# Kernel tuning notes

Measured on AMD Instinct MI355X. Metric: run time of the kernel, lower is better.

Reference implementation:

```python
import jax, jax.numpy as jnp
import numpy as np

EPS = 1e-12  # matches torch F.normalize eps


def _l2n(x, axis):
    return x / jnp.maximum(jnp.linalg.norm(x, axis=axis, keepdims=True), EPS)


def setup_inputs() -> dict:
    key = jax.random.key(0)
    k1, k2, k3 = jax.random.split(key, 3)
    x = jax.random.normal(k1, (4, 128, 30, 40), dtype=jnp.float32)
    conv_w = jax.random.normal(k2, (64, 128), dtype=jnp.float32) * 0.02  # 1x1 conv, no bias (vladv2=False)
    centroids = jax.random.uniform(k3, (64, 128), dtype=jnp.float32)
    return {"x": x, "conv_w": conv_w, "centroids": centroids}


def reference(x, conv_w, centroids):
    N, C, H, W = x.shape
    K = centroids.shape[0]
    ps, stride = 4, 1  # patch_sizes='4', strides='1'

    # descriptor-wise L2 normalization of input
    x = _l2n(x, 1)

    # 1x1 conv + softmax over clusters -> soft assignment [N,K,H,W]
    soft_assign = jax.nn.softmax(jnp.einsum('kc,nchw->nkhw', conv_w, x), axis=1)

    # weighted residuals [N,K,C,H,W] (vectorized form of the per-cluster loop)
    res = (x[:, None] - centroids[None, :, :, None, None]) * soft_assign[:, :, None]

    # global VLAD: sum over spatial, intra-norm, flatten, L2-norm
    vlad_global = res.sum(axis=(-1, -2))            # [N,K,C]
    vlad_global = _l2n(vlad_global, 2).reshape(N, K * C)
    vlad_global = _l2n(vlad_global, 1)

    # integral image over spatial dims with zero pad on top/left
    r = res.reshape(N, K * C, H, W)
    integ = jnp.cumsum(jnp.cumsum(r, axis=-1), axis=-2)
    integ = jnp.pad(integ, ((0, 0), (0, 0), (1, 0), (1, 0)))  # [N,KC,H+1,W+1]

    # dilated 2x2 box-filter conv == 4-corner integral-image lookup
    TL = integ[:, :, :H + 1 - ps:stride, :W + 1 - ps:stride]
    TR = integ[:, :, :H + 1 - ps:stride, ps::stride]
    BL = integ[:, :, ps::stride, :W + 1 - ps:stride]
    BR = integ[:, :, ps::stride, ps::stride]
    vl = (TL - TR - BL + BR) / (ps * ps)            # [N,KC,Hp,Wp]
    Hp, Wp = vl.shape[-2], vl.shape[-1]

    # local VLAD: intra-norm over descriptor dim, then global L2 per patch
    vl = vl.reshape(N, K, C, Hp * Wp)
    vl = _l2n(vl, 2).reshape(N, K * C, Hp * Wp)
    vlad_local = _l2n(vl, 1)

    return vlad_global, vlad_local
```

## Files before the change

kernel.cpp:

```cpp
#include <hip/hip_runtime.h>
#include <math.h>

#define EPSV 1e-12f

namespace {
constexpr int N_  = 4;
constexpr int C_  = 128;
constexpr int H_  = 30;
constexpr int W_  = 40;
constexpr int K_  = 64;
constexpr int HW_ = H_ * W_;
constexpr int HP_ = 27;
constexpr int WP_ = 37;
constexpr int P_  = HP_ * WP_;
constexpr int KC_ = K_ * C_;
constexpr int CP_ = C_ * P_;
constexpr int CS_ = HP_ * W_;
constexpr int SL_ = CS_ / 4;
}

static __device__ __forceinline__ float4 ld4(const float* p) {
    return *reinterpret_cast<const float4*>(p);
}

__global__ __launch_bounds__(256) void k1_norm_softmax(
    const float* __restrict__ x, const float* __restrict__ conv_w,
    float* __restrict__ xnT, float* __restrict__ xnP, float* __restrict__ sa)
{
    __shared__ float xrow[C_ * W_];
    __shared__ float conv_s[K_ * C_];
    __shared__ float invn[W_];
    __shared__ float s_s[K_ * W_];

    const int b = blockIdx.x;
    const int n = b / H_, h = b - n * H_;
    const int t = threadIdx.x;

    for (int i = t; i < C_ * W_; i += 256) {
        const int c = i / W_, w = i - c * W_;
        xrow[i] = x[(size_t)(n * C_ + c) * HW_ + h * W_ + w];
    }
    for (int i = t; i < K_ * C_; i += 256) conv_s[i] = conv_w[i];
    __syncthreads();

    if (t < W_) {
        float s = 0.f;
        for (int c = 0; c < C_; ++c) { const float v = xrow[c * W_ + t]; s += v * v; }
        invn[t] = 1.f / fmaxf(sqrtf(s), EPSV);
    }
    __syncthreads();

    for (int i = t; i < C_ * W_; i += 256) {
        const int c = i / W_, w = i - c * W_;
        const float v = xrow[i] * invn[w];
        xrow[i] = v;
        xnT[(size_t)(n * C_ + c) * HW_ + h * W_ + w] = v;
    }
    __syncthreads();

    for (int i = t; i < W_ * C_; i += 256) {
        const int w = i / C_, c = i - w * C_;
        xnP[((size_t)n * HW_ + h * W_ + w) * C_ + c] = xrow[c * W_ + w];
    }

    for (int d = t; d < K_ * W_; d += 256) {
        const int k = d / W_, w = d - k * W_;
        const float* cw = &conv_s[k * C_];
        float s = 0.f;
        for (int c = 0; c < C_; ++c) s += cw[c] * xrow[c * W_ + w];
        s_s[d] = s;
    }
    __syncthreads();

    if (t < W_) {
        const int w = t;
        float m = -1e30f;
        for (int k = 0; k < K_; ++k) m = fmaxf(m, s_s[k * W_ + w]);
        float sum = 0.f;
        for (int k = 0; k < K_; ++k) sum += expf(s_s[k * W_ + w] - m);
        const float inv = 1.f / sum;
        for (int k = 0; k < K_; ++k)
            sa[(size_t)(n * K_ + k) * HW_ + h * W_ + w] = expf(s_s[k * W_ + w] - m) * inv;
    }
}

#define COLSUM_VEC_T(cs_q, sa_s, x0, x1, x2, x3)                                \
    for (int s = t; s < SL_; s += 256) {                                        \
        const int i = s * 4;                                                    \
        const float4 sa0 = ld4(&sa_s[i]);                                       \
        const float4 sa1 = ld4(&sa_s[i + W_]);                                  \
        const float4 sa2 = ld4(&sa_s[i + 2 * W_]);                              \
        const float4 sa3 = ld4(&sa_s[i + 3 * W_]);                              \
        float acc[4][4];                                                        \
        const float* xc[4] = {x0, x1, x2, x3};                                  \
        _Pragma("unroll")                                                       \
        for (int ch = 0; ch < 4; ++ch) {                                        \
            const float4 a0 = ld4(xc[ch] + i);                                  \
            const float4 a1 = ld4(xc[ch] + i + W_);                             \
            const float4 a2 = ld4(xc[ch] + i + 2 * W_);                         \
            const float4 a3 = ld4(xc[ch] + i + 3 * W_);                         \
            acc[0][ch] = sa0.x * a0.x + sa1.x * a1.x + sa2.x * a2.x + sa3.x * a3.x; \
            acc[1][ch] = sa0.y * a0.y + sa1.y * a1.y + sa2.y * a2.y + sa3.y * a3.y; \
            acc[2][ch] = sa0.z * a0.z + sa1.z * a1.z + sa2.z * a2.z + sa3.z * a3.z; \
            acc[3][ch] = sa0.w * a0.w + sa1.w * a1.w + sa2.w * a2.w + sa3.w * a3.w; \
        }                                                                       \
        _Pragma("unroll")                                                       \
        for (int q = 0; q < 4; ++q)                                             \
            cs_q[q][s] = make_float4(acc[q][0], acc[q][1], acc[q][2], acc[q][3]); \
    }

static __device__ __forceinline__ float4 csget(const float4 cs_q[4][SL_], int e) {
    return cs_q[e & 3][e >> 2];
}

__global__ __launch_bounds__(256) void k4_merged(
    const float* __restrict__ sa, const float* __restrict__ xnT,
    const float* __restrict__ xnP, const float* __restrict__ cent,
    float* __restrict__ nsqp, float* __restrict__ vg_u,
    float* __restrict__ vg_r)
{
    __shared__ float  sa_s[HW_];
    __shared__ float  B_s[P_];
    __shared__ float4 cs_q[4][SL_];
    __shared__ float  gs[256], bss[256];
    __shared__ float  red[2];

    const int t = threadIdx.x;

    if (blockIdx.x < 256) {
        const int b = blockIdx.x;
        const int n = b >> 6, k = b & 63;
        const int c = t & 127, half = t >> 7;
        constexpr int HHW = HW_ / 2;

        const float* sarow = &sa[(size_t)b * HW_ + half * HHW];
        const float* xp = &xnP[((size_t)n * HW_ + half * HHW) * C_ + c];
        float g0 = 0.f, g1 = 0.f, g2 = 0.f, g3 = 0.f;
        float b0 = 0.f, b1 = 0.f, b2 = 0.f, b3 = 0.f;
        for (int pix = 0; pix < HHW; pix += 4) {
            const float s0 = sarow[pix + 0], s1 = sarow[pix + 1];
            const float s2 = sarow[pix + 2], s3 = sarow[pix + 3];
            g0 += s0 * xp[(size_t)(pix + 0) * C_];
            g1 += s1 * xp[(size_t)(pix + 1) * C_];
            g2 += s2 * xp[(size_t)(pix + 2) * C_];
            g3 += s3 * xp[(size_t)(pix + 3) * C_];
            b0 += s0; b1 += s1; b2 += s2; b3 += s3;
        }
        gs[t]  = (g0 + g1) + (g2 + g3);
        bss[t] = (b0 + b1) + (b2 + b3);
        __syncthreads();

        float vg = 0.f;
        if (t < 128) {
            vg = (gs[t] + gs[t + 128]) - cent[k * C_ + c] * (bss[t] + bss[t + 128]);
            float nsq = vg * vg;
            for (int off = 32; off >= 1; off >>= 1) nsq += __shfl_down(nsq, off);
            if ((t & 63) == 0) red[t >> 6] = nsq;
        }
        __syncthreads();
        const float tot  = red[0] + red[1];
        const float norm = sqrtf(tot);
        const float iv   = 1.f / fmaxf(norm, EPSV);
        if (t < 128) vg_u[(size_t)b * C_ + t] = vg * iv;
        if (t == 0) { const float rr = norm * iv; vg_r[b] = rr * rr; }
        return;
    }

    const int b  = blockIdx.x - 256;
    const int cq = b & 3;
    const int nk = b >> 2;
    const int n  = nk >> 6, k = nk & 63;

    for (int i = t; i < HW_; i += 256) sa_s[i] = sa[(size_t)nk * HW_ + i];
    __syncthreads();
    for (int p = t; p < P_; p += 256) {
        const int hp = p / WP_, wp = p - hp * WP_;
        float bs = 0.f;
#pragma unroll
        for (int dh = 0; dh < 4; ++dh) {
            const float* r = &sa_s[(hp + dh) * W_ + wp];
            bs += r[0] + r[1] + r[2] + r[3];
        }
        B_s[p] = bs;
    }

    float nsq0 = 0.f, nsq1 = 0.f, nsq2 = 0.f, nsq3 = 0.f;
    const float* xb = xnT + (size_t)n * C_ * HW_;

    for (int g = 0; g < 8; ++g) {
        const int c0 = cq * 32 + g * 4;
        const float* x0 = xb + (size_t)(c0 + 0) * HW_;
        const float* x1 = xb + (size_t)(c0 + 1) * HW_;
        const float* x2 = xb + (size_t)(c0 + 2) * HW_;
        const float* x3 = xb + (size_t)(c0 + 3) * HW_;
        __syncthreads();
        COLSUM_VEC_T(cs_q, sa_s, x0, x1, x2, x3)
        __syncthreads();
        const float4 ce = ld4(&cent[k * C_ + c0]);
#pragma unroll
        for (int pi = 0; pi < 4; ++pi) {
            const int p = t + pi * 256;
            if (p < P_) {
                const int hp = p / WP_, wp = p - hp * WP_;
                const int base = hp * W_ + wp;
                const float4 s0 = csget(cs_q, base);
                const float4 s1 = csget(cs_q, base + 1);
                const float4 s2 = csget(cs_q, base + 2);
                const float4 s3 = csget(cs_q, base + 3);
                const float Bv = B_s[p];
                const float ux = (s0.x + s1.x + s2.x + s3.x) - ce.x * Bv;
                const float uy = (s0.y + s1.y + s2.y + s3.y) - ce.y * Bv;
                const float uz = (s0.z + s1.z + s2.z + s3.z) - ce.z * Bv;
                const float uw = (s0.w + s1.w + s2.w + s3.w) - ce.w * Bv;
                const float add = ux * ux + uy * uy + uz * uz + uw * uw;
                if      (pi == 0) nsq0 += add;
                else if (pi == 1) nsq1 += add;
                else if (pi == 2) nsq2 += add;
                else              nsq3 += add;
            }
        }
    }
#pragma unroll
    for (int pi = 0; pi < 4; ++pi) {
        const int p = t + pi * 256;
        if (p < P_) {
            const float v = (pi == 0 ? nsq0 : pi == 1 ? nsq1 : pi == 2 ? nsq2 : nsq3);
            nsqp[(size_t)b * P_ + p] = v * 0.00390625f;
        }
    }
}

__global__ __launch_bounds__(256) void k5_merged(
    const float* __restrict__ nsqp, float* __restrict__ inv1,
    float* __restrict__ rloc, const float* __restrict__ vg_u,
    const float* __restrict__ vg_r, float* __restrict__ out)
{
    const int t = threadIdx.x;
    if (blockIdx.x >= 256) {
        const int n = blockIdx.x - 256;
        __shared__ float inv2s;
        if (t == 0) {
            float s = 0.f;
            for (int k = 0; k < K_; ++k) s += vg_r[n * K_ + k];
            inv2s = 1.f / fmaxf(sqrtf(s), EPSV);
        }
        __syncthreads();
        const float inv2 = inv2s;
        for (int i = t; i < KC_; i += 256)
            out[(size_t)n * KC_ + i] = vg_u[(size_t)n * KC_ + i] * inv2;
        return;
    }
    const int nk = blockIdx.x;
    for (int p = t; p < P_; p += 256) {
        const float s = nsqp[(size_t)(nk * 4 + 0) * P_ + p]
                      + nsqp[(size_t)(nk * 4 + 1) * P_ + p]
                      + nsqp[(size_t)(nk * 4 + 2) * P_ + p]
                      + nsqp[(size_t)(nk * 4 + 3) * P_ + p];
        const float norm = sqrtf(s);
        const float iv = 1.f / fmaxf(norm, EPSV);
        inv1[(size_t)nk * P_ + p] = iv * 0.0625f;
        const float rr = norm * iv;
        rloc[(size_t)nk * P_ + p] = rr * rr;
    }
}

__global__ __launch_bounds__(256) void k6_inv2(
    const float* __restrict__ rloc, float* __restrict__ inv2)
{
    const int n = blockIdx.x >> 2;
    const int p = (blockIdx.x & 3) * 256 + threadIdx.x;
    if (p < P_) {
        float s = 0.f;
        for (int k = 0; k < K_; ++k) s += rloc[(size_t)(n * K_ + k) * P_ + p];
        inv2[n * P_ + p] = 1.f / fmaxf(sqrtf(s), EPSV);
    }
}

__global__ __launch_bounds__(256) void k7_write(
    const float* __restrict__ sa, const float* __restrict__ xnT,
    const float* __restrict__ cent, const float* __restrict__ inv1,
    const float* __restrict__ inv2, float* __restrict__ outl)
{
    __shared__ float  sa_s[HW_];
    __shared__ float  scl_s[P_];
    __shared__ float  t2_s[P_];
    __shared__ float4 cs_q[4][SL_];

    const int b  = blockIdx.x;
    const int cq = b & 3;
    const int nk = b >> 2;
    const int n  = nk >> 6, k = nk & 63;
    const int t  = threadIdx.x;

    for (int i = t; i < HW_; i += 256) sa_s[i] = sa[(size_t)nk * HW_ + i];
    __syncthreads();
    for (int p = t; p < P_; p += 256) {
        const int hp = p / WP_, wp = p - hp * WP_;
        float bs = 0.f;
#pragma unroll
        for (int dh = 0; dh < 4; ++dh) {
            const float* r = &sa_s[(hp + dh) * W_ + wp];
            bs += r[0] + r[1] + r[2] + r[3];
        }
        const float sc = inv1[(size_t)nk * P_ + p] * inv2[n * P_ + p];
        scl_s[p] = sc;
        t2_s[p]  = bs * sc;
    }

    const float* xb = xnT + (size_t)n * C_ * HW_;
    float* ob = outl + (size_t)nk * CP_;

    for (int g = 0; g < 8; ++g) {
        const int m = g & 3, h8 = g >> 2;
        const int c0 = cq * 32 + h8 * 16 + m;
        const float* x0 = xb + (size_t)(c0 + 0) * HW_;
        const float* x1 = xb + (size_t)(c0 + 4) * HW_;
        const float* x2 = xb + (size_t)(c0 + 8) * HW_;
        const float* x3 = xb + (size_t)(c0 + 12) * HW_;
        __syncthreads();
        COLSUM_VEC_T(cs_q, sa_s, x0, x1, x2, x3)
        __syncthreads();
        const float ce0 = cent[k * C_ + c0];
        const float ce1 = cent[k * C_ + c0 + 4];
        const float ce2 = cent[k * C_ + c0 + 8];
        const float ce3 = cent[k * C_ + c0 + 12];
        float* ob0 = ob + (size_t)(c0 + 0) * P_;
        float* ob1 = ob + (size_t)(c0 + 4) * P_;
        float* ob2 = ob + (size_t)(c0 + 8) * P_;
        float* ob3 = ob + (size_t)(c0 + 12) * P_;

        if (t < 249) {
            const int p0 = m + t * 4;
            float4 v0, v1, v2, v3;
#pragma unroll
            for (int pi = 0; pi < 4; ++pi) {
                const int p = p0 + pi;
                const int hp = p / WP_, wp = p - hp * WP_;
                const int base = hp * W_ + wp;
                const float4 s0 = csget(cs_q, base);
                const float4 s1 = csget(cs_q, base + 1);
                const float4 s2 = csget(cs_q, base + 2);
                const float4 s3 = csget(cs_q, base + 3);
                const float sc = scl_s[p], tt = t2_s[p];
                reinterpret_cast<float*>(&v0)[pi] = (s0.x + s1.x + s2.x + s3.x) * sc - ce0 * tt;
                reinterpret_cast<float*>(&v1)[pi] = (s0.y + s1.y + s2.y + s3.y) * sc - ce1 * tt;
                reinterpret_cast<float*>(&v2)[pi] = (s0.z + s1.z + s2.z + s3.z) * sc - ce2 * tt;
                reinterpret_cast<float*>(&v3)[pi] = (s0.w + s1.w + s2.w + s3.w) * sc - ce3 * tt;
            }
            *reinterpret_cast<float4*>(ob0 + p0) = v0;
            *reinterpret_cast<float4*>(ob1 + p0) = v1;
            *reinterpret_cast<float4*>(ob2 + p0) = v2;
            *reinterpret_cast<float4*>(ob3 + p0) = v3;
        } else if (t < 252) {
            const int u = t - 249;
            const int p = (u < m) ? u : 996 + u;
            const int hp = p / WP_, wp = p - hp * WP_;
            const int base = hp * W_ + wp;
            const float4 s0 = csget(cs_q, base);
            const float4 s1 = csget(cs_q, base + 1);
            const float4 s2 = csget(cs_q, base + 2);
            const float4 s3 = csget(cs_q, base + 3);
            const float sc = scl_s[p], tt = t2_s[p];
            ob0[p] = (s0.x + s1.x + s2.x + s3.x) * sc - ce0 * tt;
            ob1[p] = (s0.y + s1.y + s2.y + s3.y) * sc - ce1 * tt;
            ob2[p] = (s0.z + s1.z + s2.z + s3.z) * sc - ce2 * tt;
            ob3[p] = (s0.w + s1.w + s2.w + s3.w) * sc - ce3 * tt;
        }
    }
}

extern "C" void kernel_launch(void* const* d_in, const int* in_sizes, int n_in,
                              void* d_out, int out_size, void* d_ws, size_t ws_size,
                              hipStream_t stream)
{
    const float* x      = (const float*)d_in[0];
    const float* conv_w = (const float*)d_in[1];
    const float* cent   = (const float*)d_in[2];
    float* out = (float*)d_out;
    float* ws  = (float*)d_ws;

    float* xnT  = ws;
    float* xnP  = ws + 614400;
    float* sa   = ws + 1228800;
    float* vg_u = ws + 1536000;
    float* vg_r = ws + 1568768;
    float* nsqp = ws + 1569024;
    float* inv1 = ws + 2592000;
    float* rloc = ws + 2847744;
    float* inv2 = ws + 3103488;

    float* outl = out + (size_t)N_ * KC_;

    k1_norm_softmax<<<N_ * H_, 256, 0, stream>>>(x, conv_w, xnT, xnP, sa);
    k4_merged<<<256 + N_ * K_ * 4, 256, 0, stream>>>(sa, xnT, xnP, cent,
                                                     nsqp, vg_u, vg_r);
    k5_merged<<<256 + N_, 256, 0, stream>>>(nsqp, inv1, rloc, vg_u, vg_r, out);
    k6_inv2<<<N_ * 4, 256, 0, stream>>>(rloc, inv2);
    k7_write<<<N_ * K_ * 4, 256, 0, stream>>>(sa, xnT, cent, inv1, inv2, outl);
}
```

Baseline: 123.1 us.

## Share sliding box-filter windows across four patches per thread and vectorize intermediates

Each thread now computes four consecutive patch outputs from a 10-element window of column sums, sharing partial sums so fewer shared-memory reads are needed than with per-patch 4-tap gathers. The B box sums in k4 move into registers the same way. Intermediate per-patch buffers are padded to a stride of 1000 so they can be read and written as float4, and k6 drops to one block per batch. In k1 the 1x1 conv is restructured around a padded transposed tile for float4 dot products. The trade-offs are more register pressure and a select at row boundaries, and k6 now runs with far fewer blocks.

```diff
diff --git a/kernel.cpp b/kernel.cpp
--- a/kernel.cpp
+++ b/kernel.cpp
@@ -13,14 +13,22 @@
 constexpr int HP_ = 27;
 constexpr int WP_ = 37;
 constexpr int P_  = HP_ * WP_;
+constexpr int PS_ = 1000;
 constexpr int KC_ = K_ * C_;
 constexpr int CP_ = C_ * P_;
 constexpr int CS_ = HP_ * W_;
 constexpr int SL_ = CS_ / 4;
+constexpr int CVP_ = 132;
 }
 
 static __device__ __forceinline__ float4 ld4(const float* p) {
     return *reinterpret_cast<const float4*>(p);
+}
+static __device__ __forceinline__ float dot4(float4 a, float4 b) {
+    return a.x * b.x + a.y * b.y + a.z * b.z + a.w * b.w;
+}
+static __device__ __forceinline__ float4 f4add(float4 a, float4 b) {
+    return make_float4(a.x + b.x, a.y + b.y, a.z + b.z, a.w + b.w);
 }
 
 __global__ __launch_bounds__(256) void k1_norm_softmax(
@@ -28,7 +36,8 @@
     float* __restrict__ xnT, float* __restrict__ xnP, float* __restrict__ sa)
 {
     __shared__ float xrow[C_ * W_];
-    __shared__ float conv_s[K_ * C_];
+    __shared__ float conv_s[K_ * CVP_];
+    __shared__ float xrowT[W_ * CVP_];
     __shared__ float invn[W_];
     __shared__ float s_s[K_ * W_];
 
@@ -40,7 +49,10 @@
         const int c = i / W_, w = i - c * W_;
         xrow[i] = x[(size_t)(n * C_ + c) * HW_ + h * W_ + w];
     }
-    for (int i = t; i < K_ * C_; i += 256) conv_s[i] = conv_w[i];
+    for (int i = t; i < K_ * C_; i += 256) {
+        const int k = i >> 7, c = i & 127;
+        conv_s[k * CVP_ + c] = conv_w[i];
+    }
     __syncthreads();
 
     if (t < W_) {
@@ -60,15 +72,39 @@
 
     for (int i = t; i < W_ * C_; i += 256) {
         const int w = i / C_, c = i - w * C_;
-        xnP[((size_t)n * HW_ + h * W_ + w) * C_ + c] = xrow[c * W_ + w];
-    }
-
-    for (int d = t; d < K_ * W_; d += 256) {
-        const int k = d / W_, w = d - k * W_;
-        const float* cw = &conv_s[k * C_];
-        float s = 0.f;
-        for (int c = 0; c < C_; ++c) s += cw[c] * xrow[c * W_ + w];
-        s_s[d] = s;
+        const float v = xrow[c * W_ + w];
+        xnP[((size_t)n * HW_ + h * W_ + w) * C_ + c] = v;
+        xrowT[w * CVP_ + c] = v;
+    }
+    __syncthreads();
+
+    {
+        const int k = t >> 2, q = t & 3;
+        float acc0 = 0.f, acc1 = 0.f, acc2 = 0.f, acc3 = 0.f, acc4 = 0.f;
+        float acc5 = 0.f, acc6 = 0.f, acc7 = 0.f, acc8 = 0.f, acc9 = 0.f;
+        const float* convk = &conv_s[k * CVP_];
+        for (int ch = 0; ch < 4; ++ch) {
+            float4 cv0 = ld4(convk + ch * 32 + 0),  cv1 = ld4(convk + ch * 32 + 4);
+            float4 cv2 = ld4(convk + ch * 32 + 8),  cv3 = ld4(convk + ch * 32 + 12);
+            float4 cv4 = ld4(convk + ch * 32 + 16), cv5 = ld4(convk + ch * 32 + 20);
+            float4 cv6 = ld4(convk + ch * 32 + 24), cv7 = ld4(convk + ch * 32 + 28);
+#pragma unroll
+            for (int wi = 0; wi < 10; ++wi) {
+                const float* xw = &xrowT[(q * 10 + wi) * CVP_ + ch * 32];
+                float s = dot4(cv0, ld4(xw)) + dot4(cv1, ld4(xw + 4))
+                        + dot4(cv2, ld4(xw + 8)) + dot4(cv3, ld4(xw + 12))
+                        + dot4(cv4, ld4(xw + 16)) + dot4(cv5, ld4(xw + 20))
+                        + dot4(cv6, ld4(xw + 24)) + dot4(cv7, ld4(xw + 28));
+                if      (wi == 0) acc0 += s; else if (wi == 1) acc1 += s;
+                else if (wi == 2) acc2 += s; else if (wi == 3) acc3 += s;
+                else if (wi == 4) acc4 += s; else if (wi == 5) acc5 += s;
+                else if (wi == 6) acc6 += s; else if (wi == 7) acc7 += s;
+                else if (wi == 8) acc8 += s; else              acc9 += s;
+            }
+        }
+        float* sd = &s_s[k * W_ + q * 10];
+        sd[0] = acc0; sd[1] = acc1; sd[2] = acc2; sd[3] = acc3; sd[4] = acc4;
+        sd[5] = acc5; sd[6] = acc6; sd[7] = acc7; sd[8] = acc8; sd[9] = acc9;
     }
     __syncthreads();
 
@@ -109,9 +145,29 @@
             cs_q[q][s] = make_float4(acc[q][0], acc[q][1], acc[q][2], acc[q][3]); \
     }
 
-static __device__ __forceinline__ float4 csget(const float4 cs_q[4][SL_], int e) {
-    return cs_q[e & 3][e >> 2];
-}
+#define WINDOW10(cs_q, b0, d, A0, A1, A2, A3)                                   \
+    {                                                                           \
+        float4 v0 = cs_q[(b0 + 0) & 3][(b0 + 0) >> 2];                          \
+        float4 v1 = cs_q[(b0 + 1) & 3][(b0 + 1) >> 2];                          \
+        float4 v2 = cs_q[(b0 + 2) & 3][(b0 + 2) >> 2];                          \
+        float4 v3 = cs_q[(b0 + 3) & 3][(b0 + 3) >> 2];                          \
+        float4 v4 = cs_q[(b0 + 4) & 3][(b0 + 4) >> 2];                          \
+        float4 v5 = cs_q[(b0 + 5) & 3][(b0 + 5) >> 2];                          \
+        float4 v6 = cs_q[(b0 + 6) & 3][(b0 + 6) >> 2];                          \
+        float4 v7 = cs_q[(b0 + 7) & 3][(b0 + 7) >> 2];                          \
+        float4 v8 = cs_q[(b0 + 8) & 3][(b0 + 8) >> 2];                          \
+        float4 v9 = cs_q[(b0 + 9) & 3][(b0 + 9) >> 2];                          \
+        const float4 t0 = f4add(v0, v1), t1 = f4add(v1, v2), t2 = f4add(v2, v3);\
+        const float4 t3 = f4add(v3, v4), t4 = f4add(v4, v5), t5 = f4add(v5, v6);\
+        const float4 t6 = f4add(v6, v7), t7 = f4add(v7, v8), t8 = f4add(v8, v9);\
+        const float4 w0 = f4add(t0, t2), w1 = f4add(t1, t3), w2 = f4add(t2, t4);\
+        const float4 w3 = f4add(t3, t5), w4 = f4add(t4, t6), w5 = f4add(t5, t7);\
+        const float4 w6 = f4add(t6, t8);                                        \
+        A0 = (0 < d) ? w0 : w3;                                                 \
+        A1 = (1 < d) ? w1 : w4;                                                 \
+        A2 = (2 < d) ? w2 : w5;                                                 \
+        A3 = (3 < d) ? w3 : w6;                                                 \
+    }
 
 __global__ __launch_bounds__(256) void k4_merged(
     const float* __restrict__ sa, const float* __restrict__ xnT,
@@ -119,9 +175,8 @@
     float* __restrict__ nsqp, float* __restrict__ vg_u,
     float* __restrict__ vg_r)
 {
-    __shared__ float  sa_s[HW_];
-    __shared__ float  B_s[P_];
-    __shared__ float4 cs_q[4][SL_];
+    __shared__ float  sa_s[HW_ + 8];
+    __shared__ float4 cs_q[4][SL_ + 1];
     __shared__ float  gs[256], bss[256];
     __shared__ float  red[2];
 
@@ -173,18 +228,32 @@
 
     for (int i = t; i < HW_; i += 256) sa_s[i] = sa[(size_t)nk * HW_ + i];
     __syncthreads();
-    for (int p = t; p < P_; p += 256) {
-        const int hp = p / WP_, wp = p - hp * WP_;
-        float bs = 0.f;
+
+    int hp0 = 0, b0 = 0, d = 4;
+    float B0 = 0.f, B1 = 0.f, B2 = 0.f, B3 = 0.f;
+    if (t < 250) {
+        const int p0 = 4 * t;
+        hp0 = p0 / WP_;
+        const int wp0 = p0 - hp0 * WP_;
+        b0 = p0 + 3 * hp0;
+        d  = WP_ - wp0;
+        const float* r0 = &sa_s[hp0 * W_ + wp0];
+        float sc[10];
 #pragma unroll
-        for (int dh = 0; dh < 4; ++dh) {
-            const float* r = &sa_s[(hp + dh) * W_ + wp];
-            bs += r[0] + r[1] + r[2] + r[3];
-        }
-        B_s[p] = bs;
-    }
-
-    float nsq0 = 0.f, nsq1 = 0.f, nsq2 = 0.f, nsq3 = 0.f;
+        for (int j = 0; j < 10; ++j)
+            sc[j] = r0[j] + r0[j + W_] + r0[j + 2 * W_] + r0[j + 3 * W_];
+        const float u0 = sc[0] + sc[1], u1 = sc[1] + sc[2], u2 = sc[2] + sc[3];
+        const float u3 = sc[3] + sc[4], u4 = sc[4] + sc[5], u5 = sc[5] + sc[6];
+        const float u6 = sc[6] + sc[7], u7 = sc[7] + sc[8], u8 = sc[8] + sc[9];
+        const float wB0 = u0 + u2, wB1 = u1 + u3, wB2 = u2 + u4;
+        const float wB3 = u3 + u5, wB4 = u4 + u6, wB5 = u5 + u7, wB6 = u6 + u8;
+        B0 = (0 < d) ? wB0 : wB3;
+        B1 = (1 < d) ? wB1 : wB4;
+        B2 = (2 < d) ? wB2 : wB5;
+        B3 = (3 < d) ? wB3 : wB6;
+    }
+
+    float4 nv0 = make_float4(0, 0, 0, 0), nv1 = nv0, nv2 = nv0, nv3 = nv0;
     const float* xb = xnT + (size_t)n * C_ * HW_;
 
     for (int g = 0; g < 8; ++g) {
@@ -196,37 +265,36 @@
         __syncthreads();
         COLSUM_VEC_T(cs_q, sa_s, x0, x1, x2, x3)
         __syncthreads();
-        const float4 ce = ld4(&cent[k * C_ + c0]);
-#pragma unroll
-        for (int pi = 0; pi < 4; ++pi) {
-            const int p = t + pi * 256;
-            if (p < P_) {
-                const int hp = p / WP_, wp = p - hp * WP_;
-                const int base = hp * W_ + wp;
-                const float4 s0 = csget(cs_q, base);
-                const float4 s1 = csget(cs_q, base + 1);
-                const float4 s2 = csget(cs_q, base + 2);
-                const float4 s3 = csget(cs_q, base + 3);
-                const float Bv = B_s[p];
-                const float ux = (s0.x + s1.x + s2.x + s3.x) - ce.x * Bv;
-                const float uy = (s0.y + s1.y + s2.y + s3.y) - ce.y * Bv;
-                const float uz = (s0.z + s1.z + s2.z + s3.z) - ce.z * Bv;
-                const float uw = (s0.w + s1.w + s2.w + s3.w) - ce.w * Bv;
-                const float add = ux * ux + uy * uy + uz * uz + uw * uw;
-                if      (pi == 0) nsq0 += add;
-                else if (pi == 1) nsq1 += add;
-                else if (pi == 2) nsq2 += add;
-                else              nsq3 += add;
-            }
-        }
-    }
-#pragma unroll
-    for (int pi = 0; pi < 4; ++pi) {
-        const int p = t + pi * 256;
-        if (p < P_) {
-            const float v = (pi == 0 ? nsq0 : pi == 1 ? nsq1 : pi == 2 ? nsq2 : nsq3);
-            nsqp[(size_t)b * P_ + p] = v * 0.00390625f;
-        }
+        if (t < 250) {
+            const float4 ce = ld4(&cent[k * C_ + c0]);
+            float4 A0, A1, A2, A3;
+            WINDOW10(cs_q, b0, d, A0, A1, A2, A3)
+            const float4 e0 = make_float4(A0.x - ce.x * B0, A0.y - ce.y * B0,
+                                          A0.z - ce.z * B0, A0.w - ce.w * B0);
+            const float4 e1 = make_float4(A1.x - ce.x * B1, A1.y - ce.y * B1,
+                                          A1.z - ce.z * B1, A1.w - ce.w * B1);
+            const float4 e2 = make_float4(A2.x - ce.x * B2, A2.y - ce.y * B2,
+                                          A2.z - ce.z * B2, A2.w - ce.w * B2);
+            const float4 e3 = make_float4(A3.x - ce.x * B3, A3.y - ce.y * B3,
+                                          A3.z - ce.z * B3, A3.w - ce.w * B3);
+            nv0 = make_float4(nv0.x + e0.x * e0.x, nv0.y + e0.y * e0.y,
+                              nv0.z + e0.z * e0.z, nv0.w + e0.w * e0.w);
+            nv1 = make_float4(nv1.x + e1.x * e1.x, nv1.y + e1.y * e1.y,
+                              nv1.z + e1.z * e1.z, nv1.w + e1.w * e1.w);
+            nv2 = make_float4(nv2.x + e2.x * e2.x, nv2.y + e2.y * e2.y,
+                              nv2.z + e2.z * e2.z, nv2.w + e2.w * e2.w);
+            nv3 = make_float4(nv3.x + e3.x * e3.x, nv3.y + e3.y * e3.y,
+                              nv3.z + e3.z * e3.z, nv3.w + e3.w * e3.w);
+        }
+    }
+    if (t < 250) {
+        const float s0 = (nv0.x + nv0.y) + (nv0.z + nv0.w);
+        const float s1 = (nv1.x + nv1.y) + (nv1.z + nv1.w);
+        const float s2 = (nv2.x + nv2.y) + (nv2.z + nv2.w);
+        const float s3 = (nv3.x + nv3.y) + (nv3.z + nv3.w);
+        *reinterpret_cast<float4*>(&nsqp[(size_t)b * PS_ + 4 * t]) =
+            make_float4(s0 * 0.00390625f, s1 * 0.00390625f,
+                        s2 * 0.00390625f, s3 * 0.00390625f);
     }
 }
 
@@ -251,28 +319,48 @@
         return;
     }
     const int nk = blockIdx.x;
-    for (int p = t; p < P_; p += 256) {
-        const float s = nsqp[(size_t)(nk * 4 + 0) * P_ + p]
-                      + nsqp[(size_t)(nk * 4 + 1) * P_ + p]
-                      + nsqp[(size_t)(nk * 4 + 2) * P_ + p]
-                      + nsqp[(size_t)(nk * 4 + 3) * P_ + p];
-        const float norm = sqrtf(s);
-        const float iv = 1.f / fmaxf(norm, EPSV);
-        inv1[(size_t)nk * P_ + p] = iv * 0.0625f;
-        const float rr = norm * iv;
-        rloc[(size_t)nk * P_ + p] = rr * rr;
+    if (t < 250) {
+        const int p0 = 4 * t;
+        const float4 a = ld4(&nsqp[(size_t)(nk * 4 + 0) * PS_ + p0]);
+        const float4 b = ld4(&nsqp[(size_t)(nk * 4 + 1) * PS_ + p0]);
+        const float4 c = ld4(&nsqp[(size_t)(nk * 4 + 2) * PS_ + p0]);
+        const float4 e = ld4(&nsqp[(size_t)(nk * 4 + 3) * PS_ + p0]);
+        float4 iv, rr;
+#pragma unroll
+        for (int j = 0; j < 4; ++j) {
+            const float s = reinterpret_cast<const float*>(&a)[j]
+                          + reinterpret_cast<const float*>(&b)[j]
+                          + reinterpret_cast<const float*>(&c)[j]
+                          + reinterpret_cast<const float*>(&e)[j];
+            const float norm = sqrtf(s);
+            const float v = 1.f / fmaxf(norm, EPSV);
+            reinterpret_cast<float*>(&iv)[j] = v * 0.0625f;
+            const float r = norm * v;
+            reinterpret_cast<float*>(&rr)[j] = r * r;
+        }
+        *reinterpret_cast<float4*>(&inv1[(size_t)nk * PS_ + p0]) = iv;
+        *reinterpret_cast<float4*>(&rloc[(size_t)nk * PS_ + p0]) = rr;
     }
 }
 
 __global__ __launch_bounds__(256) void k6_inv2(
     const float* __restrict__ rloc, float* __restrict__ inv2)
 {
-    const int n = blockIdx.x >> 2;
-    const int p = (blockIdx.x & 3) * 256 + threadIdx.x;
-    if (p < P_) {
-        float s = 0.f;
-        for (int k = 0; k < K_; ++k) s += rloc[(size_t)(n * K_ + k) * P_ + p];
-        inv2[n * P_ + p] = 1.f / fmaxf(sqrtf(s), EPSV);
+    const int n = blockIdx.x;
+    const int t = threadIdx.x;
+    if (t < 250) {
+        const int p0 = 4 * t;
+        float4 s = make_float4(0, 0, 0, 0);
+        for (int k = 0; k < K_; ++k) {
+            const float4 r = ld4(&rloc[(size_t)(n * K_ + k) * PS_ + p0]);
+            s = f4add(s, r);
+        }
+        float4 o;
+        o.x = 1.f / fmaxf(sqrtf(s.x), EPSV);
+        o.y = 1.f / fmaxf(sqrtf(s.y), EPSV);
+        o.z = 1.f / fmaxf(sqrtf(s.z), EPSV);
+        o.w = 1.f / fmaxf(sqrtf(s.w), EPSV);
+        *reinterpret_cast<float4*>(&inv2[n * PS_ + p0]) = o;
     }
 }
 
@@ -281,10 +369,10 @@
     const float* __restrict__ cent, const float* __restrict__ inv1,
     const float* __restrict__ inv2, float* __restrict__ outl)
 {
-    __shared__ float  sa_s[HW_];
+    __shared__ float  sa_s[HW_ + 8];
     __shared__ float  scl_s[P_];
     __shared__ float  t2_s[P_];
-    __shared__ float4 cs_q[4][SL_];
+    __shared__ float4 cs_q[4][SL_ + 1];
 
     const int b  = blockIdx.x;
     const int cq = b & 3;
@@ -302,7 +390,7 @@
             const float* r = &sa_s[(hp + dh) * W_ + wp];
             bs += r[0] + r[1] + r[2] + r[3];
         }
-        const float sc = inv1[(size_t)nk * P_ + p] * inv2[n * P_ + p];
+        const float sc = inv1[(size_t)nk * PS_ + p] * inv2[n * PS_ + p];
         scl_s[p] = sc;
         t2_s[p]  = bs * sc;
     }
@@ -330,36 +418,38 @@
         float* ob3 = ob + (size_t)(c0 + 12) * P_;
 
         if (t < 249) {
-            const int p0 = m + t * 4;
-            float4 v0, v1, v2, v3;
-#pragma unroll
-            for (int pi = 0; pi < 4; ++pi) {
-                const int p = p0 + pi;
-                const int hp = p / WP_, wp = p - hp * WP_;
-                const int base = hp * W_ + wp;
-                const float4 s0 = csget(cs_q, base);
-                const float4 s1 = csget(cs_q, base + 1);
-                const float4 s2 = csget(cs_q, base + 2);
-                const float4 s3 = csget(cs_q, base + 3);
-                const float sc = scl_s[p], tt = t2_s[p];
-                reinterpret_cast<float*>(&v0)[pi] = (s0.x + s1.x + s2.x + s3.x) * sc - ce0 * tt;
-                reinterpret_cast<float*>(&v1)[pi] = (s0.y + s1.y + s2.y + s3.y) * sc - ce1 * tt;
-                reinterpret_cast<float*>(&v2)[pi] = (s0.z + s1.z + s2.z + s3.z) * sc - ce2 * tt;
-                reinterpret_cast<float*>(&v3)[pi] = (s0.w + s1.w + s2.w + s3.w) * sc - ce3 * tt;
-            }
-            *reinterpret_cast<float4*>(ob0 + p0) = v0;
-            *reinterpret_cast<float4*>(ob1 + p0) = v1;
-            *reinterpret_cast<float4*>(ob2 + p0) = v2;
-            *reinterpret_cast<float4*>(ob3 + p0) = v3;
+            const int p0 = m + 4 * t;
+            const int hp0 = p0 / WP_;
+            const int wp0 = p0 - hp0 * WP_;
+            const int b0 = p0 + 3 * hp0;
+            const int d  = WP_ - wp0;
+            const float sc0 = scl_s[p0 + 0], sc1 = scl_s[p0 + 1];
+            const float sc2 = scl_s[p0 + 2], sc3 = scl_s[p0 + 3];
+            const float tt0 = t2_s[p0 + 0], tt1 = t2_s[p0 + 1];
+            const float tt2 = t2_s[p0 + 2], tt3 = t2_s[p0 + 3];
+            float4 A0, A1, A2, A3;
+            WINDOW10(cs_q, b0, d, A0, A1, A2, A3)
+            const float4 s0v = make_float4(A0.x * sc0 - ce0 * tt0, A1.x * sc1 - ce0 * tt1,
+                                           A2.x * sc2 - ce0 * tt2, A3.x * sc3 - ce0 * tt3);
+            const float4 s1v = make_float4(A0.y * sc0 - ce1 * tt0, A1.y * sc1 - ce1 * tt1,
+                                           A2.y * sc2 - ce1 * tt2, A3.y * sc3 - ce1 * tt3);
+            const float4 s2v = make_float4(A0.z * sc0 - ce2 * tt0, A1.z * sc1 - ce2 * tt1,
+                                           A2.z * sc2 - ce2 * tt2, A3.z * sc3 - ce2 * tt3);
+            const float4 s3v = make_float4(A0.w * sc0 - ce3 * tt0, A1.w * sc1 - ce3 * tt1,
+                                           A2.w * sc2 - ce3 * tt2, A3.w * sc3 - ce3 * tt3);
+            *reinterpret_cast<float4*>(ob0 + p0) = s0v;
+            *reinterpret_cast<float4*>(ob1 + p0) = s1v;
+            *reinterpret_cast<float4*>(ob2 + p0) = s2v;
+            *reinterpret_cast<float4*>(ob3 + p0) = s3v;
         } else if (t < 252) {
             const int u = t - 249;
             const int p = (u < m) ? u : 996 + u;
             const int hp = p / WP_, wp = p - hp * WP_;
             const int base = hp * W_ + wp;
-            const float4 s0 = csget(cs_q, base);
-            const float4 s1 = csget(cs_q, base + 1);
-            const float4 s2 = csget(cs_q, base + 2);
-            const float4 s3 = csget(cs_q, base + 3);
+            const float4 s0 = cs_q[(base + 0) & 3][(base + 0) >> 2];
+            const float4 s1 = cs_q[(base + 1) & 3][(base + 1) >> 2];
+            const float4 s2 = cs_q[(base + 2) & 3][(base + 2) >> 2];
+            const float4 s3 = cs_q[(base + 3) & 3][(base + 3) >> 2];
             const float sc = scl_s[p], tt = t2_s[p];
             ob0[p] = (s0.x + s1.x + s2.x + s3.x) * sc - ce0 * tt;
             ob1[p] = (s0.y + s1.y + s2.y + s3.y) * sc - ce1 * tt;
@@ -385,9 +475,9 @@
     float* vg_u = ws + 1536000;
     float* vg_r = ws + 1568768;
     float* nsqp = ws + 1569024;
-    float* inv1 = ws + 2592000;
-    float* rloc = ws + 2847744;
-    float* inv2 = ws + 3103488;
+    float* inv1 = ws + 2593024;
+    float* rloc = ws + 2849024;
+    float* inv2 = ws + 3105024;
 
     float* outl = out + (size_t)N_ * KC_;
 
@@ -395,6 +485,6 @@
     k4_merged<<<256 + N_ * K_ * 4, 256, 0, stream>>>(sa, xnT, xnP, cent,
                                                      nsqp, vg_u, vg_r);
     k5_merged<<<256 + N_, 256, 0, stream>>>(nsqp, inv1, rloc, vg_u, vg_r, out);
-    k6_inv2<<<N_ * 4, 256, 0, stream>>>(rloc, inv2);
+    k6_inv2<<<N_, 256, 0, stream>>>(rloc, inv2);
     k7_write<<<N_ * K_ * 4, 256, 0, stream>>>(sa, xnT, cent, inv1, inv2, outl);
 }
```

After: 120.2 us. -2.3%, faster.
